# Kernel tuning notes

Hardware: AMD Instinct MI355X
Metric: run time of the kernel (lower is better)

## Reference

```python
import jax, jax.numpy as jnp
import numpy as np

N = 25000      # nodes
E = 300000     # edges
IN = 32        # in_dim
EDF = 16       # edge_feat_dim
HID = 256      # hidden_dim (per-head dim, concat=False)
HEADS = 4
ACT = 16       # num_actions
G = 64         # graphs in batch
KW = 1024      # wire-mask query nodes


def setup_inputs() -> dict:
    key = jax.random.key(0)
    ks = jax.random.split(key, 20)
    def rn(k, shape, s=0.1):
        return jax.random.normal(k, shape, jnp.float32) * s
    return {
        "x": jax.random.normal(ks[0], (N, IN), jnp.float32),
        "edge_attr": jax.random.normal(ks[1], (E, EDF), jnp.float32),
        "wire_mask": jax.random.randint(ks[2], (KW,), 0, N, jnp.int32),
        "edge_index": jax.random.randint(ks[3], (2, E), 0, N, jnp.int32),
        "batch": jnp.sort(jax.random.randint(ks[4], (N,), 0, G, jnp.int32)),
        "enc_w1": rn(ks[5], (EDF, 32)),
        "enc_b1": jnp.zeros((32,), jnp.float32),
        "enc_w2": rn(ks[6], (32, IN * IN), 0.05),
        "enc_b2": jnp.zeros((IN * IN,), jnp.float32),
        "root_w": rn(ks[7], (IN, IN)),
        "nn_bias": jnp.zeros((IN,), jnp.float32),
        "gat1_w": rn(ks[8], (IN, HEADS * HID)),
        "gat1_asrc": rn(ks[9], (HEADS, HID)),
        "gat1_adst": rn(ks[10], (HEADS, HID)),
        "gat1_b": jnp.zeros((HID,), jnp.float32),
        "gat2_w": rn(ks[11], (HID, HEADS * HID)),
        "gat2_asrc": rn(ks[12], (HEADS, HID)),
        "gat2_adst": rn(ks[13], (HEADS, HID)),
        "gat2_b": jnp.zeros((HID,), jnp.float32),
        "wire_w": rn(ks[14], (HID, 1)),
        "wire_b": jnp.zeros((1,), jnp.float32),
        "act_w": rn(ks[15], (HID, ACT)),
        "act_b": jnp.zeros((ACT,), jnp.float32),
    }


def _gat(x, src, dst, W, a_src, a_dst, b):
    # PyG GATConv, concat=False (mean over heads), eval mode (no dropout),
    # self-loops already included in (src, dst).
    H, D = a_src.shape
    h = (x @ W).reshape(-1, H, D)                      # [N, H, D]
    es = (h * a_src[None]).sum(-1)                     # [N, H]
    ed = (h * a_dst[None]).sum(-1)                     # [N, H]
    e = jax.nn.leaky_relu(es[src] + ed[dst], negative_slope=0.2)  # [E2, H]
    m = jax.ops.segment_max(e, dst, num_segments=N)    # segment softmax (stable)
    w = jnp.exp(e - m[dst])
    den = jax.ops.segment_sum(w, dst, num_segments=N)
    alpha = w / (den[dst] + 1e-16)
    out = jax.ops.segment_sum(h[src] * alpha[..., None], dst, num_segments=N)
    return out.mean(axis=1) + b                        # [N, D]


def reference(x, edge_attr, wire_mask, edge_index, batch,
              enc_w1, enc_b1, enc_w2, enc_b2, root_w, nn_bias,
              gat1_w, gat1_asrc, gat1_adst, gat1_b,
              gat2_w, gat2_asrc, gat2_adst, gat2_b,
              wire_w, wire_b, act_w, act_b):
    src, dst = edge_index[0], edge_index[1]
    # NNConv (aggr='mean'): per-edge weight matrix from edge MLP
    We = (jax.nn.relu(edge_attr @ enc_w1 + enc_b1) @ enc_w2 + enc_b2)
    We = We.reshape(E, IN, IN)                         # [E, in, out]
    msg = jnp.einsum('ei,eio->eo', x[src], We)         # [E, out]
    s = jax.ops.segment_sum(msg, dst, num_segments=N)
    cnt = jax.ops.segment_sum(jnp.ones((E,), x.dtype), dst, num_segments=N)
    agg = s / jnp.maximum(cnt, 1.0)[:, None]
    h0 = jax.nn.relu(agg + x @ root_w + nn_bias)
    # GATConv default add_self_loops=True
    sl = jnp.arange(N, dtype=src.dtype)
    src2 = jnp.concatenate([src, sl])
    dst2 = jnp.concatenate([dst, sl])
    h1 = jax.nn.relu(_gat(h0, src2, dst2, gat1_w, gat1_asrc, gat1_adst, gat1_b))
    h2 = jax.nn.relu(_gat(h1, src2, dst2, gat2_w, gat2_asrc, gat2_adst, gat2_b))
    p_wire = (h2[wire_mask] @ wire_w + wire_b).squeeze(-1)   # [KW]
    pooled_s = jax.ops.segment_sum(h2, batch, num_segments=G)
    gc = jax.ops.segment_sum(jnp.ones((N,), h2.dtype), batch, num_segments=G)
    pooled = pooled_s / jnp.maximum(gc, 1.0)[:, None]        # global_mean_pool
    p_action = pooled @ act_w + act_b                        # [G, ACT]
    return (p_wire, p_action)
```

## Files before the change

kernel.cpp:

```cpp
#include <hip/hip_runtime.h>
#include <hip/hip_fp16.h>

#define N_NODES 25000
#define M_PAD   25024
#define N_TILES 1564
#define N_EDGES 300000
#define IN_DIM  32
#define EDFD    16
#define HIDD    256
#define HEADS   4
#define NACT    16
#define NGRAPH  64
#define KWIRE   1024
#define POOL_NB 64

typedef _Float16 half8v __attribute__((ext_vector_type(8)));
typedef __attribute__((ext_vector_type(4))) float f32x4;

__device__ __forceinline__ float leaky(float v) { return v > 0.f ? v : 0.2f * v; }

__global__ __launch_bounds__(256) void k_deg2(const int* __restrict__ ei,
                                              int* __restrict__ deg,
                                              int* __restrict__ deg2) {
    int e = blockIdx.x * 256 + threadIdx.x;
    if (e >= N_EDGES) return;
    atomicAdd(&deg[ei[N_EDGES + e]], 1);
    atomicAdd(&deg2[ei[e]], 1);
}

__global__ __launch_bounds__(256) void k_scan2(const int* __restrict__ degA, int* __restrict__ rpA,
                                               const int* __restrict__ degB, int* __restrict__ rpB) {
    const int* deg = blockIdx.x ? degB : degA;
    int* rowptr    = blockIdx.x ? rpB : rpA;
    __shared__ int part[256];
    int t = threadIdx.x;
    const int CH = 98;
    int base = t * CH;
    int s = 0;
    for (int i = 0; i < CH; ++i) {
        int idx = base + i;
        if (idx < N_NODES) s += deg[idx];
    }
    part[t] = s;
    __syncthreads();
    if (t == 0) {
        int run = 0;
        for (int i = 0; i < 256; ++i) { int v = part[i]; part[i] = run; run += v; }
    }
    __syncthreads();
    int run = part[t];
    for (int i = 0; i < CH; ++i) {
        int idx = base + i;
        if (idx < N_NODES) { rowptr[idx] = run; run += deg[idx]; }
    }
    if (N_NODES >= base && N_NODES < base + CH) rowptr[N_NODES] = run;
}

__global__ __launch_bounds__(256) void k_scatter2(const int* __restrict__ ei,
                                                  const float* __restrict__ ea,
                                                  const int* __restrict__ rowptr,
                                                  const int* __restrict__ rowptr2,
                                                  int* __restrict__ cursor,
                                                  int* __restrict__ cursor2,
                                                  int* __restrict__ csrc,
                                                  int* __restrict__ cdst,
                                                  int* __restrict__ posMap,
                                                  __half* __restrict__ eaP) {
    int e = blockIdx.x * 256 + threadIdx.x;
    if (e >= N_EDGES) return;
    int src = ei[e], dst = ei[N_EDGES + e];
    int p1 = atomicAdd(&cursor[dst], 1);
    int r1 = rowptr[dst] + p1;
    csrc[r1] = src;
    int p2 = atomicAdd(&cursor2[src], 1);
    int r2 = rowptr2[src] + p2;
    cdst[r2] = dst;
    posMap[r2] = r1;
    const float4* src4 = (const float4*)(ea + (size_t)e * EDFD);
    __half2* dp = (__half2*)(eaP + (size_t)r2 * EDFD);
    #pragma unroll
    for (int q = 0; q < EDFD / 4; ++q) {
        float4 v = src4[q];
        dp[q * 2]     = __float22half2_rn(make_float2(v.x, v.y));
        dp[q * 2 + 1] = __float22half2_rn(make_float2(v.z, v.w));
    }
}

__global__ __launch_bounds__(256) void k_prep(const float* __restrict__ w2,
                                              const float* __restrict__ W1,
                                              const float* __restrict__ W2,
                                              const float* __restrict__ a1s,
                                              const float* __restrict__ a1d,
                                              const float* __restrict__ a2s,
                                              const float* __restrict__ a2d,
                                              const float* __restrict__ x,
                                              const float* __restrict__ b2,
                                              const float* __restrict__ w1,
                                              __half* __restrict__ wtt,
                                              __half* __restrict__ wb1,
                                              __half* __restrict__ wb2,
                                              float* __restrict__ wa1,
                                              float* __restrict__ wd1,
                                              float* __restrict__ wa2,
                                              float* __restrict__ wd2,
                                              __half* __restrict__ xf,
                                              float* __restrict__ xb,
                                              __half* __restrict__ w1t) {
    int bid = blockIdx.x, t = threadIdx.x;
    if (bid < 128) {
        int idx = bid * 256 + t;
        int co = idx >> 5, i = idx & 31;
        wtt[idx] = __float2half(w2[(co >> 5) * 1024 + i * 32 + (co & 31)]);
    } else if (bid < 256) {
        int idx = (bid - 128) * 256 + t;
        int d = idx >> 7, k = idx & 127;
        int h = k >> 5, i = k & 31;
        wb1[idx] = __float2half(0.25f * W1[i * 1024 + h * 256 + d]);
    } else if (bid < 1280) {
        int idx = (bid - 256) * 256 + t;
        int d = idx >> 10, k = idx & 1023;
        int h = k >> 8, i = k & 255;
        wb2[idx] = __float2half(0.25f * W2[i * 1024 + h * 256 + d]);
    } else if (bid < 4405) {
        int idx = (bid - 1280) * 256 + t;
        if (idx >= N_NODES * 32) return;
        int n = idx >> 5, o = idx & 31;
        xf[idx] = __float2half(x[idx]);
        float s = 0.f;
        for (int i = 0; i < 32; ++i) s += x[n * 32 + i] * b2[i * 32 + o];
        xb[idx] = s;
    } else if (bid == 4405) {
        if (t >= 128) return;
        int h = t >> 5, i = t & 31;
        float s = 0.f, sd = 0.f;
        for (int d = 0; d < 256; ++d) {
            float w = W1[i * 1024 + h * 256 + d];
            s  += w * a1s[h * 256 + d];
            sd += w * a1d[h * 256 + d];
        }
        wa1[t] = s; wd1[t] = sd;
    } else if (bid < 4410) {
        int idx = (bid - 4406) * 256 + t;
        if (idx >= 1024) return;
        int h = idx >> 8, i = idx & 255;
        float s = 0.f, sd = 0.f;
        for (int d = 0; d < 256; ++d) {
            float w = W2[i * 1024 + h * 256 + d];
            s  += w * a2s[h * 256 + d];
            sd += w * a2d[h * 256 + d];
        }
        wa2[idx] = s; wd2[idx] = sd;
    } else {
        int idx = (bid - 4410) * 256 + t;
        if (idx >= 32 * EDFD) return;
        int j = idx >> 4, k = idx & 15;
        w1t[idx] = __float2half(w1[k * 32 + j]);
    }
}

__global__ __launch_bounds__(256) void k_msg3(const int* __restrict__ rowptr2,
                                              const int* __restrict__ posMap,
                                              const __half* __restrict__ eaP,
                                              const __half* __restrict__ w1t,
                                              const float* __restrict__ b1,
                                              const __half* __restrict__ T,
                                              const float* __restrict__ xb,
                                              __half* __restrict__ msgE) {
    int wv = threadIdx.x >> 6, lane = threadIdx.x & 63;
    int src = blockIdx.x * 4 + wv;
    if (src >= N_NODES) return;
    int r0 = rowptr2[src], r1 = rowptr2[src + 1];
    if (r0 == r1) return;
    int lr = lane & 15, lk = (lane >> 4) * 8;

    half8v bf0, bf1;
    const __half* Tp = T + (size_t)src * 1024;
    #pragma unroll
    for (int q = 0; q < 8; ++q) {
        bf0[q] = (_Float16)__half2float(Tp[(lk + q) * 32 + lr]);
        bf1[q] = (_Float16)__half2float(Tp[(lk + q) * 32 + 16 + lr]);
    }

    __half2 w1r[8][EDFD / 2];
    #pragma unroll
    for (int q = 0; q < 8; ++q) {
        const __half2* wp = (const __half2*)(w1t + (lk + q) * EDFD);
        #pragma unroll
        for (int k2 = 0; k2 < EDFD / 2; ++k2) w1r[q][k2] = wp[k2];
    }
    float b1r[8];
    #pragma unroll
    for (int q = 0; q < 8; ++q) b1r[q] = b1[lk + q];

    float xb0 = xb[src * 32 + lr], xb1 = xb[src * 32 + 16 + lr];
    int rbase = (lane >> 4) * 4;

    for (int t0 = r0; t0 < r1; t0 += 16) {
        int e = t0 + lr;
        bool ok = (e < r1);
        half8v afr;
        if (ok) {
            const __half2* ep = (const __half2*)(eaP + (size_t)e * EDFD);
            __half2 ea2[EDFD / 2];
            #pragma unroll
            for (int k2 = 0; k2 < EDFD / 2; ++k2) ea2[k2] = ep[k2];
            #pragma unroll
            for (int q = 0; q < 8; ++q) {
                float s = b1r[q];
                #pragma unroll
                for (int k2 = 0; k2 < EDFD / 2; ++k2) {
                    float2 v = __half22float2(ea2[k2]);
                    float2 w = __half22float2(w1r[q][k2]);
                    s += v.x * w.x + v.y * w.y;
                }
                afr[q] = (_Float16)fmaxf(s, 0.f);
            }
        } else {
            #pragma unroll
            for (int q = 0; q < 8; ++q) afr[q] = (_Float16)0.f;
        }
        f32x4 c0 = {0.f, 0.f, 0.f, 0.f}, c1 = {0.f, 0.f, 0.f, 0.f};
        c0 = __builtin_amdgcn_mfma_f32_16x16x32_f16(afr, bf0, c0, 0, 0, 0);
        c1 = __builtin_amdgcn_mfma_f32_16x16x32_f16(afr, bf1, c1, 0, 0, 0);
        #pragma unroll
        for (int r = 0; r < 4; ++r) {
            int er = t0 + rbase + r;
            if (er < r1) {
                int pm = posMap[er];
                msgE[(size_t)pm * 32 + lr]      = __float2half(c0[r] + xb0);
                msgE[(size_t)pm * 32 + 16 + lr] = __float2half(c1[r] + xb1);
            }
        }
    }
}

__global__ __launch_bounds__(256) void k_h0e(const float* __restrict__ x,
                                             const float* __restrict__ root_w,
                                             const float* __restrict__ nn_bias,
                                             const __half* __restrict__ msgE,
                                             const int* __restrict__ rowptr,
                                             const float* __restrict__ wa,
                                             const float* __restrict__ wd,
                                             __half* __restrict__ h0f,
                                             float* __restrict__ es,
                                             float* __restrict__ ed) {
    int t = threadIdx.x;
    int ng = t >> 5, o = t & 31;
    int n = blockIdx.x * 8 + ng;
    if (n >= N_NODES) return;
    float s = nn_bias[o];
    for (int k = 0; k < IN_DIM; ++k) s += x[n * IN_DIM + k] * root_w[k * 32 + o];
    int r0 = rowptr[n], r1 = rowptr[n + 1];
    float aggv = 0.f;
    for (int r = r0; r < r1; ++r)
        aggv += __half2float(msgE[(size_t)r * 32 + o]);
    float c = fmaxf((float)(r1 - r0), 1.f);
    s += aggv / c;
    float v = fmaxf(s, 0.f);
    h0f[n * IN_DIM + o] = __float2half(v);
    #pragma unroll
    for (int h = 0; h < 4; ++h) {
        float ss = v * wa[h * 32 + o];
        float dd = v * wd[h * 32 + o];
        #pragma unroll
        for (int off = 16; off; off >>= 1) {
            ss += __shfl_down(ss, off, 32);
            dd += __shfl_down(dd, off, 32);
        }
        if (o == 0) { es[n * 4 + h] = ss; ed[n * 4 + h] = dd; }
    }
}

__global__ __launch_bounds__(256, 2) void k_gemT(const __half* __restrict__ A,
                                                 const __half* __restrict__ Wt,
                                                 __half* __restrict__ C) {
    __shared__ __half cst[4][16 * 36];
    int t = threadIdx.x, wid = t >> 6, lane = t & 63;
    int lr = lane & 15, lk = (lane >> 4) * 8;

    int bid = blockIdx.x;
    int xcd = bid & 7, j = bid >> 3;
    int sx = j & 31;
    int y = ((j >> 5) << 3) | xcd;
    int n0 = sx * 32;

    half8v bfr[2];
    #pragma unroll
    for (int c = 0; c < 2; ++c)
        bfr[c] = *(const half8v*)(Wt + (size_t)(n0 + c * 16 + lr) * 32 + lk);

    int tb = (y * 4 + wid) * 4;
    for (int pp = 0; pp < 4; pp += 2) {
        int tA = tb + pp;
        if (tA >= N_TILES) break;
        int mA = tA * 16, mB = mA + 16;
        half8v aA = *(const half8v*)(A + (size_t)(mA + lr) * 32 + lk);
        half8v aB = *(const half8v*)(A + (size_t)(mB + lr) * 32 + lk);
        f32x4 acc[2][2];
        #pragma unroll
        for (int i = 0; i < 2; ++i)
            #pragma unroll
            for (int c = 0; c < 2; ++c)
                acc[i][c] = (f32x4){0.f, 0.f, 0.f, 0.f};
        acc[0][0] = __builtin_amdgcn_mfma_f32_16x16x32_f16(aA, bfr[0], acc[0][0], 0, 0, 0);
        acc[0][1] = __builtin_amdgcn_mfma_f32_16x16x32_f16(aA, bfr[1], acc[0][1], 0, 0, 0);
        acc[1][0] = __builtin_amdgcn_mfma_f32_16x16x32_f16(aB, bfr[0], acc[1][0], 0, 0, 0);
        acc[1][1] = __builtin_amdgcn_mfma_f32_16x16x32_f16(aB, bfr[1], acc[1][1], 0, 0, 0);

        int rbase = (lane >> 4) * 4;
        #pragma unroll
        for (int ti = 0; ti < 2; ++ti) {
            #pragma unroll
            for (int c = 0; c < 2; ++c)
                #pragma unroll
                for (int r = 0; r < 4; ++r)
                    cst[wid][(rbase + r) * 36 + c * 16 + lr] = __float2half(acc[ti][c][r]);
            int m0 = ti ? mB : mA;
            #pragma unroll
            for (int p = 0; p < 2; ++p) {
                int row = p * 8 + (lane >> 3), hb = lane & 7;
                float2 v = *(const float2*)((const char*)&cst[wid][0] + row * 72 + hb * 8);
                *(float2*)((char*)C + ((size_t)(m0 + row) * 1024 + n0) * 2 + hb * 8) = v;
            }
        }
    }
}

template <int K, typename OT>
__global__ __launch_bounds__(256, 4) void k_gemmo(const __half* __restrict__ A,
                                                  const __half* __restrict__ Wt,
                                                  const float* __restrict__ bias,
                                                  OT* __restrict__ C) {
    constexpr int CK  = 128;
    constexpr int KC  = K / CK;
    constexpr int KSC = CK / 32;
    constexpr int CB  = CK * 2;
    __shared__ __half bs[2][32 * CK];
    __shared__ float cst[4][16 * 36];
    int t = threadIdx.x, wid = t >> 6, lane = t & 63;
    int lr = lane & 15, lk = (lane >> 4) * 8;

    int bid = blockIdx.x;
    int xcd = bid & 7, rest = bid >> 3;
    int strip = rest & 7, yhi = rest >> 3;
    int y = yhi * 8 + xcd;
    if (y >= 196) return;
    int n0 = strip * 32;
    float bv0 = bias[n0 + lr], bv1 = bias[n0 + 16 + lr];
    int tb = y * 8 + wid * 2;
    int tA0 = tb     < N_TILES ? tb     : N_TILES - 1;
    int tA1 = tb + 1 < N_TILES ? tb + 1 : N_TILES - 1;
    const int swz = (lr & 7) << 4;

    f32x4 acc[2][2];
    #pragma unroll
    for (int i = 0; i < 2; ++i)
        #pragma unroll
        for (int c = 0; c < 2; ++c)
            acc[i][c] = (f32x4){0.f, 0.f, 0.f, 0.f};

    for (int i = t * 16; i < 32 * CB; i += 256 * 16) {
        int col = i / CB, offb = i % CB;
        const char* src = (const char*)Wt + ((size_t)(n0 + col) * K) * 2 + offb;
        *(float4*)((char*)bs[0] + (i ^ ((col & 7) << 4))) = *(const float4*)src;
    }
    __syncthreads();

    const __half* pA0 = A + (size_t)(tA0 * 16 + lr) * K + lk;
    const __half* pA1 = A + (size_t)(tA1 * 16 + lr) * K + lk;

    for (int kc = 0; kc < KC; ++kc) {
        int cur = kc & 1;
        if (kc + 1 < KC) {
            for (int i = t * 16; i < 32 * CB; i += 256 * 16) {
                int col = i / CB, offb = i % CB;
                const char* src = (const char*)Wt + (((size_t)(n0 + col) * K + (kc + 1) * CK) * 2 + offb);
                *(float4*)((char*)bs[cur ^ 1] + (i ^ ((col & 7) << 4))) = *(const float4*)src;
            }
        }
        half8v aH0[KSC], aH1[KSC];
        #pragma unroll
        for (int ks = 0; ks < KSC; ++ks) {
            aH0[ks] = *(const half8v*)(pA0 + kc * CK + ks * 32);
            aH1[ks] = *(const half8v*)(pA1 + kc * CK + ks * 32);
        }
        #pragma unroll
        for (int ks = 0; ks < KSC; ++ks) {
            half8v b0 = *(const half8v*)((const char*)bs[cur] + ((( 0 + lr) * CB + lk * 2 + ks * 64) ^ swz));
            half8v b1 = *(const half8v*)((const char*)bs[cur] + (((16 + lr) * CB + lk * 2 + ks * 64) ^ swz));
            acc[0][0] = __builtin_amdgcn_mfma_f32_16x16x32_f16(aH0[ks], b0, acc[0][0], 0, 0, 0);
            acc[0][1] = __builtin_amdgcn_mfma_f32_16x16x32_f16(aH0[ks], b1, acc[0][1], 0, 0, 0);
            acc[1][0] = __builtin_amdgcn_mfma_f32_16x16x32_f16(aH1[ks], b0, acc[1][0], 0, 0, 0);
            acc[1][1] = __builtin_amdgcn_mfma_f32_16x16x32_f16(aH1[ks], b1, acc[1][1], 0, 0, 0);
        }
        if (kc + 1 < KC) __syncthreads();
    }

    int rbase = (lane >> 4) * 4;
    #pragma unroll
    for (int ti = 0; ti < 2; ++ti) {
        if (tb + ti >= N_TILES) break;
        #pragma unroll
        for (int c = 0; c < 2; ++c)
            #pragma unroll
            for (int r = 0; r < 4; ++r)
                cst[wid][(rbase + r) * 36 + c * 16 + lr] =
                    fmaxf(acc[ti][c][r] + (c ? bv1 : bv0), 0.f);
        int m0 = (tb + ti) * 16;
        int row = lane >> 2, cg = lane & 3;
        const float* sp = &cst[wid][row * 36 + cg * 8];
        if constexpr (sizeof(OT) == 2) {
            __half2 o0 = __float22half2_rn(make_float2(sp[0], sp[1]));
            __half2 o1 = __float22half2_rn(make_float2(sp[2], sp[3]));
            __half2 o2 = __float22half2_rn(make_float2(sp[4], sp[5]));
            __half2 o3 = __float22half2_rn(make_float2(sp[6], sp[7]));
            float4 v = make_float4(__uint_as_float(*(unsigned*)&o0), __uint_as_float(*(unsigned*)&o1),
                                   __uint_as_float(*(unsigned*)&o2), __uint_as_float(*(unsigned*)&o3));
            *(float4*)((__half*)C + (size_t)(m0 + row) * 256 + n0 + cg * 8) = v;
        } else {
            float4 v0 = make_float4(sp[0], sp[1], sp[2], sp[3]);
            float4 v1 = make_float4(sp[4], sp[5], sp[6], sp[7]);
            float* cp = (float*)C + (size_t)(m0 + row) * 256 + n0 + cg * 8;
            *(float4*)cp = v0;
            *(float4*)(cp + 4) = v1;
        }
    }
}

__global__ __launch_bounds__(256) void k_esed2(const __half* __restrict__ h1f,
                                               const float* __restrict__ wa,
                                               const float* __restrict__ wd,
                                               float* __restrict__ es,
                                               float* __restrict__ ed) {
    int n = blockIdx.x;
    int h = threadIdx.x >> 6, lane = threadIdx.x & 63;
    float s = 0.f, d2 = 0.f;
    for (int d = lane; d < 256; d += 64) {
        float v = __half2float(h1f[(size_t)n * 256 + d]);
        s  += v * wa[h * 256 + d];
        d2 += v * wd[h * 256 + d];
    }
    #pragma unroll
    for (int off = 32; off; off >>= 1) {
        s  += __shfl_down(s, off);
        d2 += __shfl_down(d2, off);
    }
    if (lane == 0) { es[n * 4 + h] = s; ed[n * 4 + h] = d2; }
}

__global__ __launch_bounds__(256) void k_agg1(const int* __restrict__ rowptr,
                                              const int* __restrict__ csrc,
                                              const float* __restrict__ es,
                                              const float* __restrict__ ed,
                                              const __half* __restrict__ h0f,
                                              __half* __restrict__ agg0) {
    int dst = blockIdx.x * 4 + (threadIdx.x >> 6);
    if (dst >= N_NODES) return;
    int lane = threadIdx.x & 63;
    int h = lane >> 4, i2 = lane & 15;
    float edv = ed[dst * 4 + h];
    float vself = leaky(es[dst * 4 + h] + edv);
    float dn = 1.f;
    int r0 = rowptr[dst], r1 = rowptr[dst + 1];

    __half2 hv = *(const __half2*)(h0f + (size_t)dst * 32 + i2 * 2);
    float2 f = __half22float2(hv);
    float ax = f.x, ay = f.y;
    for (int r = r0; r < r1; ++r) {
        int src = csrc[r];
        float w = __expf(leaky(es[src * 4 + h] + edv) - vself);
        dn += w;
        __half2 sv = *(const __half2*)(h0f + (size_t)src * 32 + i2 * 2);
        float2 g = __half22float2(sv);
        ax += w * g.x; ay += w * g.y;
    }
    float inv = 1.f / (dn + 1e-16f);
    *(__half2*)(agg0 + (size_t)dst * 128 + h * 32 + i2 * 2) =
        __float22half2_rn(make_float2(ax * inv, ay * inv));
}

__global__ __launch_bounds__(256) void k_agg2(const int* __restrict__ rowptr,
                                              const int* __restrict__ csrc,
                                              const float* __restrict__ es,
                                              const float* __restrict__ ed,
                                              const __half* __restrict__ h1f,
                                              __half* __restrict__ agg1) {
    int dst = blockIdx.x * 4 + (threadIdx.x >> 6);
    if (dst >= N_NODES) return;
    int lane = threadIdx.x & 63;
    float vs[4], edv[4], dn[4];
    float acc[4][4];
    {
        float2 q = *(const float2*)(h1f + (size_t)dst * 256 + lane * 4);
        const __half2* hq = (const __half2*)&q;
        float2 f0 = __half22float2(hq[0]), f1 = __half22float2(hq[1]);
        #pragma unroll
        for (int h = 0; h < 4; ++h) {
            edv[h] = ed[dst * 4 + h];
            vs[h] = leaky(es[dst * 4 + h] + edv[h]);
            dn[h] = 1.f;
            acc[h][0] = f0.x; acc[h][1] = f0.y;
            acc[h][2] = f1.x; acc[h][3] = f1.y;
        }
    }
    int r0 = rowptr[dst], r1 = rowptr[dst + 1];
    for (int r = r0; r < r1; ++r) {
        int src = csrc[r];
        float4 esv = *(const float4*)(es + (size_t)src * 4);
        float w0 = __expf(leaky(esv.x + edv[0]) - vs[0]);
        float w1 = __expf(leaky(esv.y + edv[1]) - vs[1]);
        float w2 = __expf(leaky(esv.z + edv[2]) - vs[2]);
        float w3 = __expf(leaky(esv.w + edv[3]) - vs[3]);
        dn[0] += w0; dn[1] += w1; dn[2] += w2; dn[3] += w3;
        float2 q = *(const float2*)(h1f + (size_t)src * 256 + lane * 4);
        const __half2* hq = (const __half2*)&q;
        float2 f0 = __half22float2(hq[0]), f1 = __half22float2(hq[1]);
        acc[0][0] += w0 * f0.x; acc[0][1] += w0 * f0.y; acc[0][2] += w0 * f1.x; acc[0][3] += w0 * f1.y;
        acc[1][0] += w1 * f0.x; acc[1][1] += w1 * f0.y; acc[1][2] += w1 * f1.x; acc[1][3] += w1 * f1.y;
        acc[2][0] += w2 * f0.x; acc[2][1] += w2 * f0.y; acc[2][2] += w2 * f1.x; acc[2][3] += w2 * f1.y;
        acc[3][0] += w3 * f0.x; acc[3][1] += w3 * f0.y; acc[3][2] += w3 * f1.x; acc[3][3] += w3 * f1.y;
    }
    #pragma unroll
    for (int h = 0; h < 4; ++h) {
        float inv = 1.f / (dn[h] + 1e-16f);
        __half2 o0 = __float22half2_rn(make_float2(acc[h][0] * inv, acc[h][1] * inv));
        __half2 o1 = __float22half2_rn(make_float2(acc[h][2] * inv, acc[h][3] * inv));
        __half2* op = (__half2*)(agg1 + (size_t)dst * 1024 + h * 256 + lane * 4);
        op[0] = o0; op[1] = o1;
    }
}

__global__ __launch_bounds__(256) void k_wirepool(const int* __restrict__ wm,
                                                  const float* __restrict__ h2,
                                                  const float* __restrict__ ww,
                                                  const float* __restrict__ wb,
                                                  const int* __restrict__ batch,
                                                  float* __restrict__ out,
                                                  float* __restrict__ pooled,
                                                  float* __restrict__ gcnt) {
    int bid = blockIdx.x;
    if (bid < KWIRE / 4) {
        int k = bid * 4 + (threadIdx.x >> 6);
        int lane = threadIdx.x & 63;
        int n = wm[k];
        float s = 0.f;
        for (int d = lane; d < 256; d += 64) s += h2[(size_t)n * 256 + d] * ww[d];
        #pragma unroll
        for (int off = 32; off; off >>= 1) s += __shfl_down(s, off);
        if (lane == 0) out[k] = s + wb[0];
        return;
    }
    int n0 = (bid - KWIRE / 4) * POOL_NB;
    int n1 = n0 + POOL_NB; if (n1 > N_NODES) n1 = N_NODES;
    int d = threadIdx.x;
    int cur = batch[n0];
    float acc = 0.f, cnt = 0.f;
    for (int n = n0; n < n1; ++n) {
        int g = batch[n];
        if (g != cur) {
            atomicAdd(&pooled[cur * 256 + d], acc);
            if (d == 0) atomicAdd(&gcnt[cur], cnt);
            acc = 0.f; cnt = 0.f; cur = g;
        }
        acc += h2[(size_t)n * 256 + d];
        cnt += 1.f;
    }
    atomicAdd(&pooled[cur * 256 + d], acc);
    if (d == 0) atomicAdd(&gcnt[cur], cnt);
}

__global__ __launch_bounds__(256) void k_act(const float* __restrict__ pooled,
                                             const float* __restrict__ gcnt,
                                             const float* __restrict__ aw,
                                             const float* __restrict__ ab,
                                             float* __restrict__ out) {
    int u = blockIdx.x * 4 + (threadIdx.x >> 6);
    int lane = threadIdx.x & 63;
    if (u >= NGRAPH * NACT) return;
    int g = u >> 4, a = u & 15;
    float c = fmaxf(gcnt[g], 1.f);
    float s = 0.f;
    for (int d = lane; d < 256; d += 64) s += pooled[g * 256 + d] * aw[d * 16 + a];
    #pragma unroll
    for (int off = 32; off; off >>= 1) s += __shfl_down(s, off);
    if (lane == 0) out[KWIRE + u] = s / c + ab[a];
}

extern "C" void kernel_launch(void* const* d_in, const int* in_sizes, int n_in,
                              void* d_out, int out_size, void* d_ws, size_t ws_size,
                              hipStream_t stream) {
    const float* x        = (const float*)d_in[0];
    const float* edge_attr= (const float*)d_in[1];
    const int*   wire_mask= (const int*)d_in[2];
    const int*   edge_idx = (const int*)d_in[3];
    const int*   batch    = (const int*)d_in[4];
    const float* enc_w1   = (const float*)d_in[5];
    const float* enc_b1   = (const float*)d_in[6];
    const float* enc_w2   = (const float*)d_in[7];
    const float* enc_b2   = (const float*)d_in[8];
    const float* root_w   = (const float*)d_in[9];
    const float* nn_bias  = (const float*)d_in[10];
    const float* gat1_w   = (const float*)d_in[11];
    const float* gat1_asrc= (const float*)d_in[12];
    const float* gat1_adst= (const float*)d_in[13];
    const float* gat1_b   = (const float*)d_in[14];
    const float* gat2_w   = (const float*)d_in[15];
    const float* gat2_asrc= (const float*)d_in[16];
    const float* gat2_adst= (const float*)d_in[17];
    const float* gat2_b   = (const float*)d_in[18];
    const float* wire_w   = (const float*)d_in[19];
    const float* wire_b   = (const float*)d_in[20];
    const float* act_w    = (const float*)d_in[21];
    const float* act_b    = (const float*)d_in[22];
    float* out = (float*)d_out;

    float* ws = (float*)d_ws;
    size_t off = 0;
    __half* T16   = (__half*)(ws + off); off += (size_t)M_PAD * 1024 / 2;
    __half* agg1f = (__half*)(ws + off); off += (size_t)M_PAD * 1024 / 2;
    __half* agg0f = (__half*)(ws + off); off += (size_t)M_PAD * 128 / 2;
    __half* h0f   = (__half*)(ws + off); off += (size_t)M_PAD * 32 / 2;
    __half* h1f   = (__half*)(ws + off); off += (size_t)M_PAD * 256 / 2;
    __half* xf    = (__half*)(ws + off); off += (size_t)M_PAD * 32 / 2;
    __half* eaP   = (__half*)(ws + off); off += (size_t)N_EDGES * EDFD / 2;
    __half* msgE  = (__half*)(ws + off); off += (size_t)N_EDGES * 32 / 2;
    float* xb     = ws + off; off += 800000;
    float* esb    = ws + off; off += 100000;
    float* edb    = ws + off; off += 100000;
    float* h2     = ws + off; off += (size_t)M_PAD * 256;
    float* pooled = ws + off; off += NGRAPH * 256;
    float* gcnt   = ws + off; off += NGRAPH;
    int* deg      = (int*)(ws + off); off += 25600;
    int* deg2     = (int*)(ws + off); off += 25600;
    int* cursor   = (int*)(ws + off); off += 25600;
    int* cursor2  = (int*)(ws + off); off += 25600;
    int* rowptr   = (int*)(ws + off); off += 25600;
    int* rowptr2  = (int*)(ws + off); off += 25600;
    int* csrc     = (int*)(ws + off); off += N_EDGES;
    int* cdst     = (int*)(ws + off); off += N_EDGES;
    int* posMap   = (int*)(ws + off); off += N_EDGES;
    __half* wtt   = (__half*)(ws + off); off += 16384;
    __half* wb1t  = (__half*)(ws + off); off += 16384;
    __half* wb2t  = (__half*)(ws + off); off += 131072;
    __half* w1t   = (__half*)(ws + off); off += 256;
    float* wa1    = ws + off; off += 128;
    float* wd1    = ws + off; off += 128;
    float* wa2    = ws + off; off += 1024;
    float* wd2    = ws + off; off += 1024;

    const int GBT = 3328;
    const int GBO = 1600;

    hipMemsetAsync(deg, 0, 4 * 25600 * sizeof(int), stream);
    k_deg2<<<(N_EDGES + 255) / 256, 256, 0, stream>>>(edge_idx, deg, deg2);
    k_scan2<<<2, 256, 0, stream>>>(deg, rowptr, deg2, rowptr2);
    k_scatter2<<<(N_EDGES + 255) / 256, 256, 0, stream>>>(edge_idx, edge_attr, rowptr, rowptr2,
                                                          cursor, cursor2, csrc, cdst, posMap, eaP);

    k_prep<<<4412, 256, 0, stream>>>(enc_w2, gat1_w, gat2_w, gat1_asrc, gat1_adst,
                                     gat2_asrc, gat2_adst, x, enc_b2, enc_w1,
                                     wtt, wb1t, wb2t, wa1, wd1, wa2, wd2, xf, xb, w1t);

    k_gemT<<<GBT, 256, 0, stream>>>(xf, wtt, T16);
    k_msg3<<<(N_NODES + 3) / 4, 256, 0, stream>>>(rowptr2, posMap, eaP,
                                                  w1t, enc_b1, T16, xb, msgE);
    k_h0e<<<(N_NODES + 7) / 8, 256, 0, stream>>>(x, root_w, nn_bias, msgE, rowptr,
                                                 wa1, wd1, h0f, esb, edb);

    k_agg1<<<(N_NODES + 3) / 4, 256, 0, stream>>>(rowptr, csrc, esb, edb, h0f, agg0f);
    k_gemmo<128, __half><<<GBO, 256, 0, stream>>>(agg0f, wb1t, gat1_b, h1f);
    k_esed2<<<N_NODES, 256, 0, stream>>>(h1f, wa2, wd2, esb, edb);

    k_agg2<<<(N_NODES + 3) / 4, 256, 0, stream>>>(rowptr, csrc, esb, edb, h1f, agg1f);
    k_gemmo<1024, float><<<GBO, 256, 0, stream>>>(agg1f, wb2t, gat2_b, h2);

    hipMemsetAsync(pooled, 0, (NGRAPH * 256 + NGRAPH) * sizeof(float), stream);
    k_wirepool<<<KWIRE / 4 + (N_NODES + POOL_NB - 1) / POOL_NB, 256, 0, stream>>>(
        wire_mask, h2, wire_w, wire_b, batch, out, pooled, gcnt);
    k_act<<<NGRAPH * NACT / 4, 256, 0, stream>>>(pooled, gcnt, act_w, act_b, out);
}
```

Baseline: 426.7 us.

## Widen output GEMM tiles to four row tiles per wave and stage full K chunk

The output-projection GEMM now gives each wave four 16-row tiles instead of two, so each B fragment read from LDS feeds twice as many MFMAs and fewer blocks (832 instead of 1600) are launched. The B weight slab is loaded as one chunk of up to 512 K, replacing the double-buffered 128-wide chunks, and A fragments are software-pipelined two k-steps ahead. This trades more registers and LDS per block (launch bounds lowered to 3 blocks per SM) and lost overlap of B loads for less redundant B traffic and fewer barriers.

Measured after the change: 439.2 us. +2.9%, slower.

```diff
diff --git a/kernel.cpp b/kernel.cpp
--- a/kernel.cpp
+++ b/kernel.cpp
@@ -327,78 +327,86 @@
 }
 
 template <int K, typename OT>
-__global__ __launch_bounds__(256, 4) void k_gemmo(const __half* __restrict__ A,
+__global__ __launch_bounds__(256, 3) void k_gemmo(const __half* __restrict__ A,
                                                   const __half* __restrict__ Wt,
                                                   const float* __restrict__ bias,
                                                   OT* __restrict__ C) {
-    constexpr int CK  = 128;
-    constexpr int KC  = K / CK;
-    constexpr int KSC = CK / 32;
-    constexpr int CB  = CK * 2;
-    __shared__ __half bs[2][32 * CK];
+    constexpr int CK = (K > 512) ? 512 : K;
+    constexpr int NC = K / CK;
+    constexpr int RB = CK * 2;
+    constexpr int KS = CK / 32;
+    __shared__ __half bs[32 * CK];
     __shared__ float cst[4][16 * 36];
     int t = threadIdx.x, wid = t >> 6, lane = t & 63;
     int lr = lane & 15, lk = (lane >> 4) * 8;
 
     int bid = blockIdx.x;
-    int xcd = bid & 7, rest = bid >> 3;
-    int strip = rest & 7, yhi = rest >> 3;
-    int y = yhi * 8 + xcd;
-    if (y >= 196) return;
-    int n0 = strip * 32;
+    int g = (bid & 7) | ((bid >> 6) << 3);
+    int s = (bid >> 3) & 7;
+    if (g >= 98) return;
+    int n0 = s * 32;
     float bv0 = bias[n0 + lr], bv1 = bias[n0 + 16 + lr];
-    int tb = y * 8 + wid * 2;
-    int tA0 = tb     < N_TILES ? tb     : N_TILES - 1;
-    int tA1 = tb + 1 < N_TILES ? tb + 1 : N_TILES - 1;
+
+    int tb = g * 16 + wid * 4;
+    const __half* pA[4];
+    #pragma unroll
+    for (int i = 0; i < 4; ++i) {
+        int tt = tb + i < N_TILES ? tb + i : N_TILES - 1;
+        pA[i] = A + (size_t)(tt * 16 + lr) * K + lk;
+    }
     const int swz = (lr & 7) << 4;
 
-    f32x4 acc[2][2];
-    #pragma unroll
-    for (int i = 0; i < 2; ++i)
+    f32x4 acc[4][2];
+    #pragma unroll
+    for (int i = 0; i < 4; ++i)
         #pragma unroll
         for (int c = 0; c < 2; ++c)
             acc[i][c] = (f32x4){0.f, 0.f, 0.f, 0.f};
 
-    for (int i = t * 16; i < 32 * CB; i += 256 * 16) {
-        int col = i / CB, offb = i % CB;
-        const char* src = (const char*)Wt + ((size_t)(n0 + col) * K) * 2 + offb;
-        *(float4*)((char*)bs[0] + (i ^ ((col & 7) << 4))) = *(const float4*)src;
-    }
-    __syncthreads();
-
-    const __half* pA0 = A + (size_t)(tA0 * 16 + lr) * K + lk;
-    const __half* pA1 = A + (size_t)(tA1 * 16 + lr) * K + lk;
-
-    for (int kc = 0; kc < KC; ++kc) {
-        int cur = kc & 1;
-        if (kc + 1 < KC) {
-            for (int i = t * 16; i < 32 * CB; i += 256 * 16) {
-                int col = i / CB, offb = i % CB;
-                const char* src = (const char*)Wt + (((size_t)(n0 + col) * K + (kc + 1) * CK) * 2 + offb);
-                *(float4*)((char*)bs[cur ^ 1] + (i ^ ((col & 7) << 4))) = *(const float4*)src;
+    for (int ch = 0; ch < NC; ++ch) {
+        if (ch) __syncthreads();
+        for (int i = t * 16; i < 32 * RB; i += 256 * 16) {
+            int col = i / RB, offb = i % RB;
+            const char* src = (const char*)Wt + ((size_t)(n0 + col) * K + ch * CK) * 2 + offb;
+            *(float4*)((char*)bs + (i ^ ((col & 7) << 4))) = *(const float4*)src;
+        }
+        __syncthreads();
+
+        const char* bp0 = (const char*)bs + (size_t)lr * RB;
+        const char* bp1 = (const char*)bs + (size_t)(16 + lr) * RB;
+        int ko = ch * CK;
+
+        half8v a0[4], a1[4];
+        #pragma unroll
+        for (int i = 0; i < 4; ++i) a0[i] = *(const half8v*)(pA[i] + ko);
+
+        for (int ks = 0; ks < KS; ks += 2) {
+            #pragma unroll
+            for (int i = 0; i < 4; ++i) a1[i] = *(const half8v*)(pA[i] + ko + (ks + 1) * 32);
+            half8v b0 = *(const half8v*)(bp0 + ((ks * 64 + lk * 2) ^ swz));
+            half8v b1 = *(const half8v*)(bp1 + ((ks * 64 + lk * 2) ^ swz));
+            #pragma unroll
+            for (int i = 0; i < 4; ++i) {
+                acc[i][0] = __builtin_amdgcn_mfma_f32_16x16x32_f16(a0[i], b0, acc[i][0], 0, 0, 0);
+                acc[i][1] = __builtin_amdgcn_mfma_f32_16x16x32_f16(a0[i], b1, acc[i][1], 0, 0, 0);
             }
-        }
-        half8v aH0[KSC], aH1[KSC];
-        #pragma unroll
-        for (int ks = 0; ks < KSC; ++ks) {
-            aH0[ks] = *(const half8v*)(pA0 + kc * CK + ks * 32);
-            aH1[ks] = *(const half8v*)(pA1 + kc * CK + ks * 32);
-        }
-        #pragma unroll
-        for (int ks = 0; ks < KSC; ++ks) {
-            half8v b0 = *(const half8v*)((const char*)bs[cur] + ((( 0 + lr) * CB + lk * 2 + ks * 64) ^ swz));
-            half8v b1 = *(const half8v*)((const char*)bs[cur] + (((16 + lr) * CB + lk * 2 + ks * 64) ^ swz));
-            acc[0][0] = __builtin_amdgcn_mfma_f32_16x16x32_f16(aH0[ks], b0, acc[0][0], 0, 0, 0);
-            acc[0][1] = __builtin_amdgcn_mfma_f32_16x16x32_f16(aH0[ks], b1, acc[0][1], 0, 0, 0);
-            acc[1][0] = __builtin_amdgcn_mfma_f32_16x16x32_f16(aH1[ks], b0, acc[1][0], 0, 0, 0);
-            acc[1][1] = __builtin_amdgcn_mfma_f32_16x16x32_f16(aH1[ks], b1, acc[1][1], 0, 0, 0);
-        }
-        if (kc + 1 < KC) __syncthreads();
+            if (ks + 2 < KS) {
+                #pragma unroll
+                for (int i = 0; i < 4; ++i) a0[i] = *(const half8v*)(pA[i] + ko + (ks + 2) * 32);
+            }
+            half8v c0 = *(const half8v*)(bp0 + (((ks + 1) * 64 + lk * 2) ^ swz));
+            half8v c1 = *(const half8v*)(bp1 + (((ks + 1) * 64 + lk * 2) ^ swz));
+            #pragma unroll
+            for (int i = 0; i < 4; ++i) {
+                acc[i][0] = __builtin_amdgcn_mfma_f32_16x16x32_f16(a1[i], c0, acc[i][0], 0, 0, 0);
+                acc[i][1] = __builtin_amdgcn_mfma_f32_16x16x32_f16(a1[i], c1, acc[i][1], 0, 0, 0);
+            }
+        }
     }
 
     int rbase = (lane >> 4) * 4;
     #pragma unroll
-    for (int ti = 0; ti < 2; ++ti) {
+    for (int ti = 0; ti < 4; ++ti) {
         if (tb + ti >= N_TILES) break;
         #pragma unroll
         for (int c = 0; c < 2; ++c)
@@ -649,7 +657,7 @@
     float* wd2    = ws + off; off += 1024;
 
     const int GBT = 3328;
-    const int GBO = 1600;
+    const int GBO = 832;
 
     hipMemsetAsync(deg, 0, 4 * 25600 * sizeof(int), stream);
     k_deg2<<<(N_EDGES + 255) / 256, 256, 0, stream>>>(edge_idx, deg, deg2);
```

## Fuse layer-2 attention score projections into the layer-1 GEMM epilogue

Applied to the files above, without the earlier changes.

Removes the separate k_esed2 kernel, which re-read the fp16 layer-1 output to compute per-head source and destination attention scores. The GEMM epilogue now computes partial dot products per 32-column strip from the staged fp32 tile and accumulates them into fresh zeroed buffers with atomicAdd. This saves one launch and one full pass over h1. The cost is many global float atomics (one per strip, head and score per row), an extra memset, and a non-deterministic summation order.

Measured after the change: 421.0 us. No clear change (-1.3%).

```diff
diff --git a/kernel.cpp b/kernel.cpp
--- a/kernel.cpp
+++ b/kernel.cpp
@@ -326,11 +326,15 @@
     }
 }
 
-template <int K, typename OT>
+template <int K, typename OT, bool FUSE_ED>
 __global__ __launch_bounds__(256, 4) void k_gemmo(const __half* __restrict__ A,
                                                   const __half* __restrict__ Wt,
                                                   const float* __restrict__ bias,
-                                                  OT* __restrict__ C) {
+                                                  OT* __restrict__ C,
+                                                  const float* __restrict__ wa,
+                                                  const float* __restrict__ wd,
+                                                  float* __restrict__ es,
+                                                  float* __restrict__ ed) {
     constexpr int CK  = 128;
     constexpr int KC  = K / CK;
     constexpr int KSC = CK / 32;
@@ -424,28 +428,26 @@
             *(float4*)cp = v0;
             *(float4*)(cp + 4) = v1;
         }
-    }
-}
-
-__global__ __launch_bounds__(256) void k_esed2(const __half* __restrict__ h1f,
-                                               const float* __restrict__ wa,
-                                               const float* __restrict__ wd,
-                                               float* __restrict__ es,
-                                               float* __restrict__ ed) {
-    int n = blockIdx.x;
-    int h = threadIdx.x >> 6, lane = threadIdx.x & 63;
-    float s = 0.f, d2 = 0.f;
-    for (int d = lane; d < 256; d += 64) {
-        float v = __half2float(h1f[(size_t)n * 256 + d]);
-        s  += v * wa[h * 256 + d];
-        d2 += v * wd[h * 256 + d];
-    }
-    #pragma unroll
-    for (int off = 32; off; off >>= 1) {
-        s  += __shfl_down(s, off);
-        d2 += __shfl_down(d2, off);
-    }
-    if (lane == 0) { es[n * 4 + h] = s; ed[n * 4 + h] = d2; }
+        if constexpr (FUSE_ED) {
+            int rowg = m0 + row;
+            #pragma unroll
+            for (int h = 0; h < 4; ++h) {
+                float pes = 0.f, ped = 0.f;
+                #pragma unroll
+                for (int d = 0; d < 8; ++d) {
+                    float vv = sp[d];
+                    pes += vv * wa[h * 256 + n0 + cg * 8 + d];
+                    ped += vv * wd[h * 256 + n0 + cg * 8 + d];
+                }
+                pes += __shfl_down(pes, 1, 4); pes += __shfl_down(pes, 2, 4);
+                ped += __shfl_down(ped, 1, 4); ped += __shfl_down(ped, 2, 4);
+                if (cg == 0 && rowg < N_NODES) {
+                    atomicAdd(&es[rowg * 4 + h], pes);
+                    atomicAdd(&ed[rowg * 4 + h], ped);
+                }
+            }
+        }
+    }
 }
 
 __global__ __launch_bounds__(256) void k_agg1(const int* __restrict__ rowptr,
@@ -647,11 +649,14 @@
     float* wd1    = ws + off; off += 128;
     float* wa2    = ws + off; off += 1024;
     float* wd2    = ws + off; off += 1024;
+    float* esb2   = ws + off; off += 100000;
+    float* edb2   = ws + off; off += 100000;
 
     const int GBT = 3328;
     const int GBO = 1600;
 
     hipMemsetAsync(deg, 0, 4 * 25600 * sizeof(int), stream);
+    hipMemsetAsync(esb2, 0, 2 * 100000 * sizeof(float), stream);
     k_deg2<<<(N_EDGES + 255) / 256, 256, 0, stream>>>(edge_idx, deg, deg2);
     k_scan2<<<2, 256, 0, stream>>>(deg, rowptr, deg2, rowptr2);
     k_scatter2<<<(N_EDGES + 255) / 256, 256, 0, stream>>>(edge_idx, edge_attr, rowptr, rowptr2,
@@ -668,11 +673,12 @@
                                                  wa1, wd1, h0f, esb, edb);
 
     k_agg1<<<(N_NODES + 3) / 4, 256, 0, stream>>>(rowptr, csrc, esb, edb, h0f, agg0f);
-    k_gemmo<128, __half><<<GBO, 256, 0, stream>>>(agg0f, wb1t, gat1_b, h1f);
-    k_esed2<<<N_NODES, 256, 0, stream>>>(h1f, wa2, wd2, esb, edb);
-
-    k_agg2<<<(N_NODES + 3) / 4, 256, 0, stream>>>(rowptr, csrc, esb, edb, h1f, agg1f);
-    k_gemmo<1024, float><<<GBO, 256, 0, stream>>>(agg1f, wb2t, gat2_b, h2);
+    k_gemmo<128, __half, true><<<GBO, 256, 0, stream>>>(agg0f, wb1t, gat1_b, h1f,
+                                                        wa2, wd2, esb2, edb2);
+
+    k_agg2<<<(N_NODES + 3) / 4, 256, 0, stream>>>(rowptr, csrc, esb2, edb2, h1f, agg1f);
+    k_gemmo<1024, float, false><<<GBO, 256, 0, stream>>>(agg1f, wb2t, gat2_b, h2,
+                                                         nullptr, nullptr, nullptr, nullptr);
 
     hipMemsetAsync(pooled, 0, (NGRAPH * 256 + NGRAPH) * sizeof(float), stream);
     k_wirepool<<<KWIRE / 4 + (N_NODES + POOL_NB - 1) / POOL_NB, 256, 0, stream>>>(
```
